# Performance work log

Hardware: AMD Instinct MI355X
Metric: run time of the kernel (lower is better)

## Reference

```python
import jax, jax.numpy as jnp
import numpy as np

B, N, DIM, PDIM, H, DH, M, CDIM = 1, 48, 256, 128, 8, 64, 128, 512
INNER = H * DH
EPS = 1e-5


def setup_inputs() -> dict:
    key = jax.random.key(0)
    ks = jax.random.split(key, 40)
    def w(k, shape):
        return jax.random.normal(k, shape, jnp.float32) * 0.02
    inp = {
        "singles": jax.random.normal(ks[0], (B, N, DIM), jnp.float32),
        "pairs": jax.random.normal(ks[1], (B, N, N, PDIM), jnp.float32),
        "ligand_emb": jax.random.normal(ks[2], (B, M, CDIM), jnp.float32),
        "mask": jnp.ones((B, N), dtype=bool),
        "rotary_pos": jax.random.normal(ks[3], (1, 1, 1, DH), jnp.float32),
        "ln_s_g": jnp.ones((DIM,)), "ln_s_b": jnp.zeros((DIM,)),
        "ln_p_g": jnp.ones((PDIM,)), "ln_p_b": jnp.zeros((PDIM,)),
        "sa_qkv": w(ks[4], (DIM, 3 * INNER)),
        "sa_out_w": w(ks[5], (INNER, DIM)), "sa_out_b": jnp.zeros((DIM,)),
        "sff_w1": w(ks[6], (DIM, 4 * DIM)), "sff_b1": jnp.zeros((4 * DIM,)),
        "sff_w2": w(ks[7], (4 * DIM, DIM)), "sff_b2": jnp.zeros((DIM,)),
        "pa_qkv": w(ks[8], (PDIM, 3 * INNER)),
        "pa_out_w": w(ks[9], (INNER, PDIM)), "pa_out_b": jnp.zeros((PDIM,)),
        "pff_w1": w(ks[10], (PDIM, 4 * PDIM)), "pff_b1": jnp.zeros((4 * PDIM,)),
        "pff_w2": w(ks[11], (4 * PDIM, PDIM)), "pff_b2": jnp.zeros((PDIM,)),
        "ca_q": w(ks[12], (PDIM, INNER)),
        "ca_kv": w(ks[13], (CDIM, 2 * INNER)),
        "ca_out_w": w(ks[14], (INNER, PDIM)), "ca_out_b": jnp.zeros((PDIM,)),
        "s2p_w": w(ks[15], (DIM, PDIM)), "s2p_b": jnp.zeros((PDIM,)),
        "p2s_w": w(ks[16], (PDIM, DIM)), "p2s_b": jnp.zeros((DIM,)),
    }
    return inp


def _rotate_half(x):
    shp = x.shape
    xr = x.reshape(shp[:-1] + (shp[-1] // 2, 2))
    x1, x2 = xr[..., 0], xr[..., 1]
    return jnp.stack((-x2, x1), axis=-1).reshape(shp)


def _rope(pos, t):
    return t * jnp.cos(pos) + _rotate_half(t) * jnp.sin(pos)


def _split_heads(t):
    b, n, _ = t.shape
    return t.reshape(b, n, H, DH).transpose(0, 2, 1, 3)  # b h n d


def _merge_heads(t):
    b, h, n, d = t.shape
    return t.transpose(0, 2, 1, 3).reshape(b, n, h * d)


def _layer_norm(x, g, b):
    m = jnp.mean(x, axis=-1, keepdims=True)
    v = jnp.mean(jnp.square(x - m), axis=-1, keepdims=True)
    return (x - m) * jax.lax.rsqrt(v + EPS) * g + b


def _mish(x):
    return x * jnp.tanh(jax.nn.softplus(x))


def _attn_core(q, k, v, key_mask=None):
    dots = jnp.einsum('bhid,bhjd->bhij', q, k) * (DH ** -0.5)
    if key_mask is not None:
        neg = -jnp.finfo(dots.dtype).max
        dots = jnp.where(key_mask[:, None, None, :], dots, neg)
    a = jax.nn.softmax(dots, axis=-1)
    return jnp.einsum('bhij,bhjd->bhid', a, v)


def _self_attn(x, w_qkv, w_out, b_out, rotary_pos, key_mask=None):
    q, k, v = jnp.split(x @ w_qkv, 3, axis=-1)
    q, k, v = _split_heads(q), _split_heads(k), _split_heads(v)
    q, k = _rope(rotary_pos, q), _rope(rotary_pos, k)
    out = _merge_heads(_attn_core(q, k, v, key_mask))
    return out @ w_out + b_out


def _cross_attn(x, ctx, w_q, w_kv, w_out, b_out, rotary_pos):
    q = _split_heads(x @ w_q)
    k, v = jnp.split(ctx @ w_kv, 2, axis=-1)
    k, v = _split_heads(k), _split_heads(v)
    q, k = _rope(rotary_pos, q), _rope(rotary_pos, k)
    out = _merge_heads(_attn_core(q, k, v))
    return out @ w_out + b_out


def _ff(x, w1, b1, w2, b2):
    return _mish(x @ w1 + b1) @ w2 + b2


def _forward(singles, pairs, ligand_emb, mask, rotary_pos,
             ln_s_g, ln_s_b, ln_p_g, ln_p_b,
             sa_qkv, sa_out_w, sa_out_b, sff_w1, sff_b1, sff_w2, sff_b2,
             pa_qkv, pa_out_w, pa_out_b, pff_w1, pff_b1, pff_w2, pff_b2,
             ca_q, ca_kv, ca_out_w, ca_out_b, s2p_w, s2p_b, p2s_w, p2s_b):
    # single track
    s_norm = _layer_norm(singles, ln_s_g, ln_s_b)
    singles = singles + _self_attn(s_norm, sa_qkv, sa_out_w, sa_out_b, rotary_pos, mask)
    singles = singles + _ff(singles, sff_w1, sff_b1, sff_w2, sff_b2)
    # pair track: flatten i*j into one long sequence
    b, i, j, d = pairs.shape
    p_norm = _layer_norm(pairs, ln_p_g, ln_p_b)
    p_flat = p_norm.reshape(b, i * j, d)
    p_attn = _self_attn(p_flat, pa_qkv, pa_out_w, pa_out_b, rotary_pos, None)
    pairs = pairs + p_attn.reshape(b, i, j, d)
    # ligand cross attention (on pre-norm pairs, as in source)
    p_cross = _cross_attn(p_flat, ligand_emb, ca_q, ca_kv, ca_out_w, ca_out_b, rotary_pos)
    pairs = pairs + p_cross.reshape(b, i, j, d)
    pairs = pairs + _ff(pairs, pff_w1, pff_b1, pff_w2, pff_b2)
    # cross-track communication
    single_contrib = singles @ s2p_w + s2p_b              # [b,n,pdim]
    pair_contrib = jnp.mean(pairs, axis=2) @ p2s_w + p2s_b  # [b,n,dim]
    pairs = pairs + single_contrib[:, None, :, :] + single_contrib[:, :, None, :]
    singles = singles + pair_contrib
    return singles, pairs


def reference(singles, pairs, ligand_emb, mask, rotary_pos,
              ln_s_g, ln_s_b, ln_p_g, ln_p_b,
              sa_qkv, sa_out_w, sa_out_b, sff_w1, sff_b1, sff_w2, sff_b2,
              pa_qkv, pa_out_w, pa_out_b, pff_w1, pff_b1, pff_w2, pff_b2,
              ca_q, ca_kv, ca_out_w, ca_out_b, s2p_w, s2p_b, p2s_w, p2s_b):
    return _forward(singles, pairs, ligand_emb, mask, rotary_pos,
                    ln_s_g, ln_s_b, ln_p_g, ln_p_b,
                    sa_qkv, sa_out_w, sa_out_b, sff_w1, sff_b1, sff_w2, sff_b2,
                    pa_qkv, pa_out_w, pa_out_b, pff_w1, pff_b1, pff_w2, pff_b2,
                    ca_q, ca_kv, ca_out_w, ca_out_b, s2p_w, s2p_b, p2s_w, p2s_b)
```

## Files before the change

### kernel.cpp

```cpp
#include <hip/hip_runtime.h>
#include <math.h>

#define EPS 1e-5f

typedef __attribute__((ext_vector_type(8))) short short8;
typedef __attribute__((ext_vector_type(4))) short short4v;
typedef __attribute__((ext_vector_type(4))) float float4v;

__device__ inline short f2bf(float f) {
  union { float f; unsigned u; } c; c.f = f;
  unsigned u = c.u;
  u += 0x7FFF + ((u >> 16) & 1);
  return (short)(u >> 16);
}

struct TransDesc { const float* src; short* dst; int K; int N; int tile0; };
struct TransArgs { TransDesc d[13]; int nd; };

__global__ __launch_bounds__(256) void prep_kernel(
    TransArgs args, int tiles, int ln_end,
    const float* __restrict__ xs, const float* __restrict__ gs,
    const float* __restrict__ bs, float* __restrict__ ys,
    const float* __restrict__ xp, const float* __restrict__ gp,
    const float* __restrict__ bp, float* __restrict__ yp,
    float* __restrict__ zbase) {
  int bid = blockIdx.x;
  int tid = threadIdx.x;
  if (bid < tiles) {
    __shared__ float tile[32][33];
    int wi = 0;
    while (wi + 1 < args.nd && args.d[wi + 1].tile0 <= bid) ++wi;
    TransDesc de = args.d[wi];
    int lt = bid - de.tile0;
    int ntx = de.N / 32;
    int k0 = (lt / ntx) * 32, n0 = (lt % ntx) * 32;
    int tx = tid & 31, ty = tid >> 5;
#pragma unroll
    for (int yy = 0; yy < 4; ++yy) {
      int kk = ty + yy * 8;
      tile[kk][tx] = de.src[(size_t)(k0 + kk) * de.N + n0 + tx];
    }
    __syncthreads();
#pragma unroll
    for (int yy = 0; yy < 4; ++yy) {
      int nn = ty + yy * 8;
      de.dst[(size_t)(n0 + nn) * de.K + k0 + tx] = f2bf(tile[tx][nn]);
    }
    return;
  }
  if (bid < ln_end) {
    __shared__ float red[256];
    int row = bid - tiles;
    const float *x, *g, *b;
    float* y;
    int D;
    if (row < 48) { x = xs; g = gs; b = bs; y = ys; D = 256; }
    else { row -= 48; x = xp; g = gp; b = bp; y = yp; D = 128; }
    const float* xr = x + (size_t)row * D;
    float* yr = y + (size_t)row * D;
    float s = (tid < D) ? xr[tid] : 0.f;
    red[tid] = s; __syncthreads();
    for (int st = 128; st > 0; st >>= 1) {
      if (tid < st) red[tid] += red[tid + st];
      __syncthreads();
    }
    float mean = red[0] / D;
    __syncthreads();
    float v = 0.f;
    if (tid < D) { float t = xr[tid] - mean; v = t * t; }
    red[tid] = v; __syncthreads();
    for (int st = 128; st > 0; st >>= 1) {
      if (tid < st) red[tid] += red[tid + st];
      __syncthreads();
    }
    float rstd = rsqrtf(red[0] / D + EPS);
    if (tid < D) yr[tid] = (xr[tid] - mean) * rstd * g[tid] + b[tid];
    return;
  }
  size_t i4 = ((size_t)(bid - ln_end) * 256 + tid) * 4;
  *(float4*)(zbase + i4) = make_float4(0.f, 0.f, 0.f, 0.f);
}

struct ProjJob {
  const float* A; const short* Wt;
  int M, K, N;
  short *Qd, *Kd, *Vd;
  int rowspad, vld, qend, kend, tile0;
  float qscale;
};
struct ProjArgs { ProjJob j[4]; int nj; };

__global__ __launch_bounds__(256) void proj_kernel(
    ProjArgs args, const float* __restrict__ rope_pos) {
  __shared__ short As[64][72];
  __shared__ short Ws[64][72];
  int t = blockIdx.x;
  int ji = 0;
  while (ji + 1 < args.nj && args.j[ji + 1].tile0 <= t) ++ji;
  ProjJob jb = args.j[ji];
  int lt = t - jb.tile0;
  int ntx = jb.N / 64;
  int m0 = (lt / ntx) * 64, n0 = (lt % ntx) * 64;
  int tid = threadIdx.x;
  int wave = tid >> 6, lane = tid & 63;
  int n16 = lane & 15, quad = lane >> 4;
  float4v acc[4];
#pragma unroll
  for (int f = 0; f < 4; ++f) acc[f] = (float4v){0.f, 0.f, 0.f, 0.f};

  for (int k0 = 0; k0 < jb.K; k0 += 64) {
    __syncthreads();
    for (int idx = tid; idx < 1024; idx += 256) {
      int row = idx >> 4, c4 = (idx & 15) * 4;
      float4 av = make_float4(0.f, 0.f, 0.f, 0.f);
      if (m0 + row < jb.M)
        av = *(const float4*)(jb.A + (size_t)(m0 + row) * jb.K + k0 + c4);
      short4v s;
      s.x = f2bf(av.x); s.y = f2bf(av.y); s.z = f2bf(av.z); s.w = f2bf(av.w);
      *(short4v*)&As[row][c4] = s;
    }
    for (int idx = tid; idx < 512; idx += 256) {
      int row = idx >> 3, kc = (idx & 7) * 8;
      short8 w = *(const short8*)(jb.Wt + (size_t)(n0 + row) * jb.K + k0 + kc);
      *(short8*)&Ws[row][kc] = w;
    }
    __syncthreads();
#pragma unroll
    for (int s = 0; s < 2; ++s) {
      short8 a = *(const short8*)&As[wave * 16 + n16][s * 32 + quad * 8];
#pragma unroll
      for (int f = 0; f < 4; ++f) {
        short8 b = *(const short8*)&Ws[f * 16 + n16][s * 32 + quad * 8];
        acc[f] = __builtin_amdgcn_mfma_f32_16x16x32_bf16(a, b, acc[f], 0, 0, 0);
      }
    }
  }

#pragma unroll
  for (int f = 0; f < 4; ++f) {
    int col = n0 + f * 16 + n16;
    if (col < jb.kend) {
      int rel = (col < jb.qend) ? col : col - jb.qend;
      int hh = rel >> 6, d = col & 63;
      float pv = rope_pos[d];
      float cp = cosf(pv), sp = sinf(pv);
      float sc = (col < jb.qend) ? jb.qscale : 1.f;
      short* dst = (col < jb.qend) ? jb.Qd : jb.Kd;
#pragma unroll
      for (int r = 0; r < 4; ++r) {
        float x = acc[f][r];
        float xp = __shfl_xor(x, 1);
        float o = (n16 & 1) ? (x * cp + xp * sp) : (x * cp - xp * sp);
        int row = m0 + wave * 16 + quad * 4 + r;
        if (row < jb.M)
          dst[((size_t)hh * jb.rowspad + row) * 64 + d] = f2bf(o * sc);
      }
    } else {
      int vcol = col - jb.kend;
      int hh = vcol >> 6, d = vcol & 63;
      short4v s;
#pragma unroll
      for (int r = 0; r < 4; ++r) ((short*)&s)[r] = f2bf(acc[f][r]);
      int j0 = m0 + wave * 16 + quad * 4;
      if (j0 < jb.M)
        *(short4v*)(jb.Vd + (size_t)(hh * 64 + d) * jb.vld + j0) = s;
    }
  }
}

struct FJob {
  const short *Q, *K, *V;
  int nkpad;
  float* O;
  float* Lsum;
  int nq, nk, ns, nqt, blk0;
};
struct FArgs { FJob j[3]; int nj; };

__global__ __launch_bounds__(256) void fattn_kernel(FArgs args) {
  __shared__ short Ks[64][72];
  __shared__ short Vs[64][72];
  __shared__ short Ps[4][16][72];
  int bid = blockIdx.x;
  int ji = 0;
  while (ji + 1 < args.nj && args.j[ji + 1].blk0 <= bid) ++ji;
  FJob jb = args.j[ji];
  int local = bid - jb.blk0;
  int h = local & 7;
  int rest = local >> 3;
  int qt = rest % jb.nqt;
  int z = rest / jb.nqt;
  int nqpad = jb.nqt * 64;
  int q0 = qt * 64;
  int nkpad = jb.nkpad, nk = jb.nk;
  int tid = threadIdx.x;
  int wave = tid >> 6, lane = tid & 63;
  int n16 = lane & 15, quad = lane >> 4;

  int ntiles = nkpad >> 6;
  int tiles_per = (ntiles + jb.ns - 1) / jb.ns;
  int kbeg = z * tiles_per * 64;
  int kend = min(nkpad, kbeg + tiles_per * 64);

  const short* kb = jb.K + (size_t)h * nkpad * 64;
  const short* vt = jb.V + (size_t)h * 64 * nkpad;
  const short* qr = jb.Q + (size_t)h * nqpad * 64 +
                    (size_t)(q0 + wave * 16 + n16) * 64;
  short8 a0 = *(const short8*)(qr + quad * 8);
  short8 a1 = *(const short8*)(qr + 32 + quad * 8);

  float4v Of[4];
#pragma unroll
  for (int f = 0; f < 4; ++f) Of[f] = (float4v){0.f, 0.f, 0.f, 0.f};
  float l_par[4] = {0.f, 0.f, 0.f, 0.f};

  int r0 = tid >> 3, cc0 = (tid & 7) * 8;
  int r1 = (tid + 256) >> 3, cc1 = ((tid + 256) & 7) * 8;

  short8 pK0 = *(const short8*)(kb + (size_t)(kbeg + r0) * 64 + cc0);
  short8 pK1 = *(const short8*)(kb + (size_t)(kbeg + r1) * 64 + cc1);
  short8 pV0 = *(const short8*)(vt + (size_t)r0 * nkpad + kbeg + cc0);
  short8 pV1 = *(const short8*)(vt + (size_t)r1 * nkpad + kbeg + cc1);

  for (int kt0 = kbeg; kt0 < kend; kt0 += 64) {
    __syncthreads();
    *(short8*)&Ks[r0][cc0] = pK0;
    *(short8*)&Ks[r1][cc1] = pK1;
    *(short8*)&Vs[r0][cc0] = pV0;
    *(short8*)&Vs[r1][cc1] = pV1;
    int nxt = kt0 + 64;
    if (nxt < kend) {
      pK0 = *(const short8*)(kb + (size_t)(nxt + r0) * 64 + cc0);
      pK1 = *(const short8*)(kb + (size_t)(nxt + r1) * 64 + cc1);
      pV0 = *(const short8*)(vt + (size_t)r0 * nkpad + nxt + cc0);
      pV1 = *(const short8*)(vt + (size_t)r1 * nkpad + nxt + cc1);
    }
    __syncthreads();

    float4v Sf[4];
#pragma unroll
    for (int f = 0; f < 4; ++f) {
      short8 b0 = *(const short8*)&Ks[f * 16 + n16][quad * 8];
      short8 b1 = *(const short8*)&Ks[f * 16 + n16][32 + quad * 8];
      float4v a = (float4v){0.f, 0.f, 0.f, 0.f};
      a = __builtin_amdgcn_mfma_f32_16x16x32_bf16(a0, b0, a, 0, 0, 0);
      a = __builtin_amdgcn_mfma_f32_16x16x32_bf16(a1, b1, a, 0, 0, 0);
      Sf[f] = a;
    }
    if (kt0 + 64 > nk) {
#pragma unroll
      for (int f = 0; f < 4; ++f) {
        int j = kt0 + f * 16 + n16;
        if (j >= nk) {
          Sf[f][0] = -1e30f; Sf[f][1] = -1e30f;
          Sf[f][2] = -1e30f; Sf[f][3] = -1e30f;
        }
      }
    }
    float p[4][4];
#pragma unroll
    for (int r = 0; r < 4; ++r) {
      float t = 0.f;
#pragma unroll
      for (int f = 0; f < 4; ++f) {
        float e = __expf(Sf[f][r]);
        p[f][r] = e;
        t += e;
      }
      l_par[r] += t;
    }
#pragma unroll
    for (int f = 0; f < 4; ++f)
#pragma unroll
      for (int r = 0; r < 4; ++r)
        Ps[wave][quad * 4 + r][f * 16 + n16] = f2bf(p[f][r]);
#pragma unroll
    for (int s = 0; s < 2; ++s) {
      short8 pa = *(const short8*)&Ps[wave][n16][s * 32 + quad * 8];
#pragma unroll
      for (int f = 0; f < 4; ++f) {
        short8 vb = *(const short8*)&Vs[f * 16 + n16][s * 32 + quad * 8];
        Of[f] = __builtin_amdgcn_mfma_f32_16x16x32_bf16(pa, vb, Of[f], 0, 0, 0);
      }
    }
  }

  float l[4];
#pragma unroll
  for (int r = 0; r < 4; ++r) {
    float t = l_par[r];
    t += __shfl_xor(t, 1);
    t += __shfl_xor(t, 2);
    t += __shfl_xor(t, 4);
    t += __shfl_xor(t, 8);
    l[r] = t;
  }

  if (jb.ns == 1) {
#pragma unroll
    for (int r = 0; r < 4; ++r) {
      int row = q0 + wave * 16 + quad * 4 + r;
      if (row >= jb.nq) continue;
      float inv = 1.f / l[r];
#pragma unroll
      for (int f = 0; f < 4; ++f)
        jb.O[(size_t)row * 512 + h * 64 + f * 16 + n16] = Of[f][r] * inv;
    }
  } else {
#pragma unroll
    for (int r = 0; r < 4; ++r) {
      int row = q0 + wave * 16 + quad * 4 + r;
#pragma unroll
      for (int f = 0; f < 4; ++f)
        atomicAdd(&jb.O[(size_t)row * 512 + h * 64 + f * 16 + n16], Of[f][r]);
      if (n16 == 0) atomicAdd(&jb.Lsum[(size_t)h * jb.nq + row], l[r]);
    }
  }
}

struct TJob {
  int type;
  const float *A1, *A2;
  const short *W1, *W2;
  const float *b1, *b2, *resid, *normL;
  float *C, *pmean;
  short* Ct;
  int M, K1, K2, N, nz, mish, dual, tile0;
};
struct TArgs { TJob j[4]; int nj; };

__global__ __launch_bounds__(256) void tjobs_kernel(TArgs args) {
  __shared__ short As[32][136];
  __shared__ short Ws[32][136];
  int t = blockIdx.x;
  int ji = 0;
  while (ji + 1 < args.nj && args.j[ji + 1].tile0 <= t) ++ji;
  TJob jb = args.j[ji];
  int lt = t - jb.tile0;
  int tid = threadIdx.x;

  if (jb.type == 2) {
    int idx = lt * 256 + tid;
    int d = idx & 127;
    int j = (idx >> 7) % 48;
    int i = idx / (48 * 128);
    jb.C[idx] = jb.A1[idx] + jb.A2[j * 128 + d] + jb.A2[i * 128 + d];
    return;
  }
  if (jb.type == 4) {
    if (tid < 128) {
      float acc = jb.b1[tid];
      for (int m = 0; m < jb.K1; ++m)
        acc += jb.A1[m] * jb.resid[(size_t)m * 128 + tid];
      jb.C[tid] = acc;
    }
    return;
  }

  int ntx = jb.N / 32, nmt = (jb.M + 31) >> 5;
  int per_z = ntx * nmt;
  int z = lt / per_z, rem = lt - z * per_z;
  int m0 = (rem / ntx) * 32, n0 = (rem % ntx) * 32;
  int wave = tid >> 6, lane = tid & 63;
  int n16 = lane & 15, quad = lane >> 4;
  int mrow = (wave >> 1) * 16, ncol = (wave & 1) * 16;
  float4v acc = (float4v){0.f, 0.f, 0.f, 0.f};
  int Ktot = jb.K1 + (jb.dual ? jb.K2 : 0);
  int chunk = Ktot / jb.nz;
  int kst = z * chunk, ken = kst + chunk;
  for (int kc = kst; kc < ken; kc += 128) {
    __syncthreads();
    for (int idx = tid; idx < 1024; idx += 256) {
      int row = idx >> 5, c4 = (idx & 31) * 4;
      int k = kc + c4;
      float4 av = make_float4(0.f, 0.f, 0.f, 0.f);
      if (m0 + row < jb.M) {
        if (!jb.dual || k < jb.K1) {
          av = *(const float4*)(jb.A1 + (size_t)(m0 + row) * jb.K1 + k);
          if (jb.normL) {
            float inv = 1.f / jb.normL[(size_t)(k >> 6) * jb.M + m0 + row];
            av.x *= inv; av.y *= inv; av.z *= inv; av.w *= inv;
          }
        } else {
          av = *(const float4*)(jb.A2 + (size_t)(m0 + row) * jb.K2 +
                                (k - jb.K1));
        }
      }
      short4v s;
      s.x = f2bf(av.x); s.y = f2bf(av.y); s.z = f2bf(av.z); s.w = f2bf(av.w);
      *(short4v*)&As[row][c4] = s;
    }
    for (int idx = tid; idx < 512; idx += 256) {
      int row = idx >> 4, k8 = (idx & 15) * 8;
      int k = kc + k8;
      const short* src = (jb.dual && k >= jb.K1)
          ? (jb.W2 + (size_t)(n0 + row) * jb.K2 + (k - jb.K1))
          : (jb.W1 + (size_t)(n0 + row) * jb.K1 + k);
      *(short8*)&Ws[row][k8] = *(const short8*)src;
    }
    __syncthreads();
#pragma unroll
    for (int ks = 0; ks < 4; ++ks) {
      short8 a = *(const short8*)&As[mrow + n16][ks * 32 + quad * 8];
      short8 b = *(const short8*)&Ws[ncol + n16][ks * 32 + quad * 8];
      acc = __builtin_amdgcn_mfma_f32_16x16x32_bf16(a, b, acc, 0, 0, 0);
    }
  }
  int col = n0 + ncol + n16;
  if (jb.Ct) {
    short4v s;
#pragma unroll
    for (int r = 0; r < 4; ++r) ((short*)&s)[r] = f2bf(acc[r]);
    int rbase = m0 + mrow + quad * 4;
    *(short4v*)(jb.Ct + (size_t)col * jb.M + rbase) = s;
    return;
  }
  if (jb.nz == 1) {
#pragma unroll
    for (int r = 0; r < 4; ++r) {
      int row = m0 + mrow + quad * 4 + r;
      if (row >= jb.M) continue;
      float v = acc[r];
      if (jb.b1) v += jb.b1[col];
      if (jb.b2) v += jb.b2[col];
      if (jb.mish) {
        float sp = (v > 20.f) ? v : log1pf(expf(v));
        v = v * tanhf(sp);
      }
      if (jb.resid) v += jb.resid[(size_t)row * jb.N + col];
      jb.C[(size_t)row * jb.N + col] = v;
      if (jb.pmean) atomicAdd(&jb.pmean[(row / 48) * 128 + col], v * (1.f / 48.f));
    }
  } else {
#pragma unroll
    for (int r = 0; r < 4; ++r) {
      int row = m0 + mrow + quad * 4 + r;
      if (row >= jb.M) continue;
      float v = acc[r];
      if (z == 0) {
        if (jb.b1) v += jb.b1[col];
        if (jb.b2) v += jb.b2[col];
        if (jb.resid) v += jb.resid[(size_t)row * jb.N + col];
      }
      atomicAdd(&jb.C[(size_t)row * jb.N + col], v);
      if (jb.pmean) atomicAdd(&jb.pmean[(row / 48) * 128 + col], v * (1.f / 48.f));
    }
  }
}

extern "C" void kernel_launch(void* const* d_in, const int* in_sizes, int n_in,
                              void* d_out, int out_size, void* d_ws, size_t ws_size,
                              hipStream_t stream) {
  (void)in_sizes; (void)n_in; (void)out_size; (void)ws_size;
  const float* singles = (const float*)d_in[0];
  const float* pairs   = (const float*)d_in[1];
  const float* ligand  = (const float*)d_in[2];
  const float* rotary  = (const float*)d_in[4];
  const float* ln_s_g  = (const float*)d_in[5];
  const float* ln_s_b  = (const float*)d_in[6];
  const float* ln_p_g  = (const float*)d_in[7];
  const float* ln_p_b  = (const float*)d_in[8];
  const float* sa_out_b= (const float*)d_in[11];
  const float* sff_b1  = (const float*)d_in[13];
  const float* sff_w2f = (const float*)d_in[14];
  const float* sff_b2  = (const float*)d_in[15];
  const float* pa_out_b= (const float*)d_in[18];
  const float* pff_b1  = (const float*)d_in[20];
  const float* pff_b2  = (const float*)d_in[22];
  const float* ca_out_b= (const float*)d_in[26];
  const float* s2p_wf  = (const float*)d_in[27];
  const float* s2p_b   = (const float*)d_in[28];
  const float* p2s_b   = (const float*)d_in[30];

  float* ws = (float*)d_ws;
  size_t off = 0;
  auto alloc = [&](size_t n) { float* p = ws + off; off += n; return p; };
  float* s_norm   = alloc(12288);
  float* p_norm   = alloc(294912);
  float* attn_s   = alloc(24576);
  float* h1_s     = alloc(49152);
  float* attn_c   = alloc(1179648);
  float* attn_p   = alloc(1179648);
  float* Lsum     = alloc(18432);
  float* pairs2   = alloc(294912);
  float* pairs3   = alloc(294912);
  float* singles1 = alloc(12288);
  float* singles2 = alloc(12288);
  float* sc_buf   = alloc(6144);
  float* pmean    = alloc(6144);
  const size_t zero_floats = 1824768;
  float* bc       = alloc(128);
  short* Wct      = (short*)alloc(65536);
  short* wt       = (short*)alloc(1081344);
  short* Qb       = (short*)alloc(589824);
  short* Kb       = (short*)alloc(589824);
  short* Vtb      = (short*)alloc(589824);
  short* Qcb      = (short*)alloc(589824);
  short* Kcb      = (short*)alloc(32768);
  short* Vcb      = (short*)alloc(32768);
  short* Qsb      = (short*)alloc(16384);
  short* Ksb      = (short*)alloc(16384);
  short* Vsb      = (short*)alloc(16384);

  float* out_s = (float*)d_out;
  float* out_p = (float*)d_out + 12288;

  struct WSpec { const float* src; int K, N; };
  WSpec specs[13] = {
    {(const float*)d_in[9], 256, 1536}, {(const float*)d_in[10], 512, 256},
    {(const float*)d_in[12], 256, 1024}, {sff_w2f, 1024, 256},
    {(const float*)d_in[16], 128, 1536}, {(const float*)d_in[17], 512, 128},
    {(const float*)d_in[19], 128, 512}, {(const float*)d_in[21], 512, 128},
    {(const float*)d_in[23], 128, 512}, {(const float*)d_in[24], 512, 1024},
    {(const float*)d_in[25], 512, 128}, {s2p_wf, 256, 128},
    {(const float*)d_in[29], 128, 256}};
  TransArgs ta;
  ta.nd = 13;
  short* wptr[13];
  int tiles = 0;
  size_t woff = 0;
  for (int i = 0; i < 13; ++i) {
    ta.d[i].src = specs[i].src;
    ta.d[i].dst = wt + woff;
    ta.d[i].K = specs[i].K;
    ta.d[i].N = specs[i].N;
    ta.d[i].tile0 = tiles;
    wptr[i] = wt + woff;
    woff += (size_t)specs[i].K * specs[i].N;
    tiles += (specs[i].K / 32) * (specs[i].N / 32);
  }

  const float scale = 0.125f;
  const int NS = 4;

  {
    int ln_end = tiles + 48 + 2304;
    int zero_blocks = (int)(zero_floats / 1024);
    hipLaunchKernelGGL(prep_kernel, dim3(ln_end + zero_blocks), dim3(256), 0,
                       stream, ta, tiles, ln_end,
                       singles, ln_s_g, ln_s_b, s_norm,
                       pairs, ln_p_g, ln_p_b, p_norm, attn_p);
  }

  {
    ProjArgs pa;
    pa.nj = 4;
    int t0 = 0;
    auto setj = [&](int i, const float* A, const short* Wt, int M, int K,
                    int N, short* Qd, short* Kd, short* Vd, int rowspad,
                    int vld, int qend, int kend, float qscale) {
      pa.j[i] = {A, Wt, M, K, N, Qd, Kd, Vd, rowspad, vld, qend, kend, t0,
                 qscale};
      t0 += (N / 64) * ((M + 63) / 64);
    };
    setj(0, s_norm, wptr[0], 48, 256, 1536, Qsb, Ksb, Vsb, 64, 64, 512, 1024,
         scale);
    setj(1, p_norm, wptr[4], 2304, 128, 1536, Qb, Kb, Vtb, 2304, 2304, 512,
         1024, scale);
    setj(2, p_norm, wptr[8], 2304, 128, 512, Qcb, nullptr, nullptr, 2304, 0,
         512, 512, scale);
    setj(3, ligand, wptr[9], 128, 512, 1024, nullptr, Kcb, Vcb, 128, 128, 0,
         512, 1.f);
    hipLaunchKernelGGL(proj_kernel, dim3(t0), dim3(256), 0, stream, pa, rotary);
  }

  {
    FArgs fa;
    fa.nj = 3;
    fa.j[0] = {Qb, Kb, Vtb, 2304, attn_p, Lsum, 2304, 2304, NS, 36, 0};
    fa.j[1] = {Qsb, Ksb, Vsb, 64, attn_s, nullptr, 48, 48, 1, 1, 8 * 36 * NS};
    fa.j[2] = {Qcb, Kcb, Vcb, 128, attn_c, nullptr, 2304, 128, 1, 36,
               8 * 36 * NS + 8};
    hipLaunchKernelGGL(fattn_kernel, dim3(8 * 36 * NS + 8 + 8 * 36), dim3(256),
                       0, stream, fa);
  }

  auto gemm_tiles = [](int M, int N, int nz) {
    return (N / 32) * ((M + 31) / 32) * nz;
  };
  TJob jz{};

  {
    TArgs tj; tj.nj = 4;
    TJob a = jz;
    a.type = 0; a.A1 = attn_p; a.A2 = attn_c; a.W1 = wptr[5]; a.W2 = wptr[10];
    a.b1 = pa_out_b; a.b2 = ca_out_b; a.resid = pairs; a.normL = Lsum;
    a.C = pairs2; a.M = 2304; a.K1 = 512; a.K2 = 512; a.N = 128; a.nz = 4;
    a.dual = 1; a.tile0 = 0;
    int t1 = gemm_tiles(2304, 128, 4);
    TJob b = jz;
    b.type = 0; b.A1 = attn_s; b.W1 = wptr[1]; b.b1 = sa_out_b;
    b.resid = singles; b.C = singles1; b.M = 48; b.K1 = 512; b.N = 256;
    b.nz = 2; b.tile0 = t1;
    int t2 = t1 + gemm_tiles(48, 256, 2);
    TJob c = jz;
    c.type = 0; c.A1 = sff_w2f; c.W1 = wptr[11]; c.Ct = Wct;
    c.M = 1024; c.K1 = 256; c.N = 128; c.nz = 1; c.tile0 = t2;
    int t3 = t2 + gemm_tiles(1024, 128, 1);
    TJob d = jz;
    d.type = 4; d.A1 = sff_b2; d.b1 = s2p_b; d.resid = s2p_wf; d.C = bc;
    d.K1 = 256; d.tile0 = t3;
    tj.j[0] = a; tj.j[1] = b; tj.j[2] = c; tj.j[3] = d;
    hipLaunchKernelGGL(tjobs_kernel, dim3(t3 + 1), dim3(256), 0, stream, tj);
  }
  {
    TArgs tj; tj.nj = 2;
    TJob a = jz;
    a.type = 0; a.A1 = pairs2; a.W1 = wptr[6]; a.b1 = pff_b1; a.mish = 1;
    a.C = attn_c ; a.M = 2304; a.K1 = 128; a.N = 512; a.nz = 1;
    a.tile0 = 0;
    int t1 = gemm_tiles(2304, 512, 1);
    TJob b = jz;
    b.type = 0; b.A1 = singles1; b.W1 = wptr[2]; b.b1 = sff_b1; b.mish = 1;
    b.C = h1_s; b.M = 48; b.K1 = 256; b.N = 1024; b.nz = 1; b.tile0 = t1;
    tj.j[0] = a; tj.j[1] = b;
    hipLaunchKernelGGL(tjobs_kernel, dim3(t1 + gemm_tiles(48, 1024, 1)),
                       dim3(256), 0, stream, tj);
  }
  {
    TArgs tj; tj.nj = 3;
    TJob a = jz;
    a.type = 0; a.A1 = attn_c ; a.W1 = wptr[7]; a.b1 = pff_b2;
    a.resid = pairs2; a.C = pairs3; a.pmean = pmean;
    a.M = 2304; a.K1 = 512; a.N = 128; a.nz = 2; a.tile0 = 0;
    int t1 = gemm_tiles(2304, 128, 2);
    TJob b = jz;
    b.type = 0; b.A1 = h1_s; b.W1 = wptr[3]; b.b1 = sff_b2; b.resid = singles1;
    b.C = singles2; b.M = 48; b.K1 = 1024; b.N = 256; b.nz = 2; b.tile0 = t1;
    int t2 = t1 + gemm_tiles(48, 256, 2);
    TJob c = jz;
    c.type = 0; c.A1 = singles1; c.A2 = h1_s; c.W1 = wptr[11]; c.W2 = Wct;
    c.b1 = bc; c.C = sc_buf; c.M = 48; c.K1 = 256; c.K2 = 1024; c.N = 128;
    c.nz = 2; c.dual = 1; c.tile0 = t2;
    tj.j[0] = a; tj.j[1] = b; tj.j[2] = c;
    hipLaunchKernelGGL(tjobs_kernel, dim3(t2 + gemm_tiles(48, 128, 2)),
                       dim3(256), 0, stream, tj);
  }
  {
    TArgs tj; tj.nj = 2;
    TJob a = jz;
    a.type = 0; a.A1 = pmean; a.W1 = wptr[12]; a.b1 = p2s_b;
    a.resid = singles2; a.C = out_s; a.M = 48; a.K1 = 128; a.N = 256;
    a.nz = 1; a.tile0 = 0;
    int t1 = gemm_tiles(48, 256, 1);
    TJob b = jz;
    b.type = 2; b.A1 = pairs3; b.A2 = sc_buf; b.C = out_p; b.tile0 = t1;
    tj.j[0] = a; tj.j[1] = b;
    hipLaunchKernelGGL(tjobs_kernel, dim3(t1 + 1152), dim3(256), 0, stream, tj);
  }
}
```

Before: 288.9 us.

## Replace split-KV atomic accumulation with bf16 partial buffers and combine pass

The pair-attention split-KV blocks now write unnormalized bf16 partial outputs and row sums into per-split buffers instead of issuing fp32 atomicAdds into a zeroed output. A new combine job sums the partials and normalizes. The out-projection GEMMs shift one launch later, which adds an extra kernel launch. Separately, the pair-mean atomics are pre-reduced across each wave with shuffles so each column issues one atomic, and the large zero-init region shrinks. The trade-off is lower precision in the partials plus extra memory traffic and a launch, in exchange for removing heavy atomic contention and memset work.

Result: no change. 287.6 us (-0.4%).

```diff
diff --git a/kernel.cpp b/kernel.cpp
--- a/kernel.cpp
+++ b/kernel.cpp
@@ -12,6 +12,11 @@
   unsigned u = c.u;
   u += 0x7FFF + ((u >> 16) & 1);
   return (short)(u >> 16);
+}
+__device__ inline float bf2f(short s) {
+  union { unsigned u; float f; } c;
+  c.u = ((unsigned)(unsigned short)s) << 16;
+  return c.f;
 }
 
 struct TransDesc { const float* src; short* dst; int K; int N; int tile0; };
@@ -172,7 +177,7 @@
   const short *Q, *K, *V;
   int nkpad;
   float* O;
-  float* Lsum;
+  short* Opart; float* Lpart;
   int nq, nk, ns, nqt, blk0;
 };
 struct FArgs { FJob j[3]; int nj; };
@@ -307,13 +312,15 @@
         jb.O[(size_t)row * 512 + h * 64 + f * 16 + n16] = Of[f][r] * inv;
     }
   } else {
+    size_t pbase = ((size_t)(h * jb.nqt + qt) * jb.ns + z);
+    short* op = jb.Opart + pbase * 4096;
 #pragma unroll
     for (int r = 0; r < 4; ++r) {
-      int row = q0 + wave * 16 + quad * 4 + r;
+      int rl = wave * 16 + quad * 4 + r;
 #pragma unroll
       for (int f = 0; f < 4; ++f)
-        atomicAdd(&jb.O[(size_t)row * 512 + h * 64 + f * 16 + n16], Of[f][r]);
-      if (n16 == 0) atomicAdd(&jb.Lsum[(size_t)h * jb.nq + row], l[r]);
+        op[(size_t)rl * 64 + f * 16 + n16] = f2bf(Of[f][r]);
+      if (n16 == 0) jb.Lpart[pbase * 64 + rl] = l[r];
     }
   }
 }
@@ -322,7 +329,7 @@
   int type;
   const float *A1, *A2;
   const short *W1, *W2;
-  const float *b1, *b2, *resid, *normL;
+  const float *b1, *b2, *resid, *L;
   float *C, *pmean;
   short* Ct;
   int M, K1, K2, N, nz, mish, dual, tile0;
@@ -353,6 +360,35 @@
       for (int m = 0; m < jb.K1; ++m)
         acc += jb.A1[m] * jb.resid[(size_t)m * 128 + tid];
       jb.C[tid] = acc;
+    }
+    return;
+  }
+  if (jb.type == 5) {
+    int h = lt / jb.M, qt = lt % jb.M;
+    int q = tid >> 2, d0 = (tid & 3) * 16;
+    size_t base = (size_t)(h * jb.M + qt) * jb.nz;
+    float l = 0.f;
+    for (int s = 0; s < jb.nz; ++s) l += jb.L[(base + s) * 64 + q];
+    float inv = 1.f / l;
+    float acc[16];
+#pragma unroll
+    for (int i = 0; i < 16; ++i) acc[i] = 0.f;
+    for (int s = 0; s < jb.nz; ++s) {
+      const short* op = jb.Ct + (base + s) * 4096 + q * 64 + d0;
+#pragma unroll
+      for (int c = 0; c < 2; ++c) {
+        short8 v = *(const short8*)(op + c * 8);
+#pragma unroll
+        for (int j = 0; j < 8; ++j) acc[c * 8 + j] += bf2f(v[j]);
+      }
+    }
+    int row = qt * 64 + q;
+    float* dst = jb.C + (size_t)row * 512 + h * 64 + d0;
+#pragma unroll
+    for (int c = 0; c < 4; ++c) {
+      float4 o = make_float4(acc[c * 4] * inv, acc[c * 4 + 1] * inv,
+                             acc[c * 4 + 2] * inv, acc[c * 4 + 3] * inv);
+      *(float4*)(dst + c * 4) = o;
     }
     return;
   }
@@ -375,16 +411,11 @@
       int k = kc + c4;
       float4 av = make_float4(0.f, 0.f, 0.f, 0.f);
       if (m0 + row < jb.M) {
-        if (!jb.dual || k < jb.K1) {
+        if (!jb.dual || k < jb.K1)
           av = *(const float4*)(jb.A1 + (size_t)(m0 + row) * jb.K1 + k);
-          if (jb.normL) {
-            float inv = 1.f / jb.normL[(size_t)(k >> 6) * jb.M + m0 + row];
-            av.x *= inv; av.y *= inv; av.z *= inv; av.w *= inv;
-          }
-        } else {
+        else
           av = *(const float4*)(jb.A2 + (size_t)(m0 + row) * jb.K2 +
                                 (k - jb.K1));
-        }
       }
       short4v s;
       s.x = f2bf(av.x); s.y = f2bf(av.y); s.z = f2bf(av.z); s.w = f2bf(av.w);
@@ -415,6 +446,7 @@
     *(short4v*)(jb.Ct + (size_t)col * jb.M + rbase) = s;
     return;
   }
+  float tsum = 0.f;
   if (jb.nz == 1) {
 #pragma unroll
     for (int r = 0; r < 4; ++r) {
@@ -429,7 +461,7 @@
       }
       if (jb.resid) v += jb.resid[(size_t)row * jb.N + col];
       jb.C[(size_t)row * jb.N + col] = v;
-      if (jb.pmean) atomicAdd(&jb.pmean[(row / 48) * 128 + col], v * (1.f / 48.f));
+      tsum += v;
     }
   } else {
 #pragma unroll
@@ -443,8 +475,15 @@
         if (jb.resid) v += jb.resid[(size_t)row * jb.N + col];
       }
       atomicAdd(&jb.C[(size_t)row * jb.N + col], v);
-      if (jb.pmean) atomicAdd(&jb.pmean[(row / 48) * 128 + col], v * (1.f / 48.f));
-    }
+      tsum += v;
+    }
+  }
+  if (jb.pmean) {
+    tsum *= (1.f / 48.f);
+    tsum += __shfl_xor(tsum, 16);
+    tsum += __shfl_xor(tsum, 32);
+    if (quad == 0)
+      atomicAdd(&jb.pmean[((m0 + mrow) / 48) * 128 + col], tsum);
   }
 }
 
@@ -479,18 +518,19 @@
   float* p_norm   = alloc(294912);
   float* attn_s   = alloc(24576);
   float* h1_s     = alloc(49152);
+  float* attn_p   = alloc(294912);
   float* attn_c   = alloc(1179648);
-  float* attn_p   = alloc(1179648);
-  float* Lsum     = alloc(18432);
   float* pairs2   = alloc(294912);
   float* pairs3   = alloc(294912);
   float* singles1 = alloc(12288);
   float* singles2 = alloc(12288);
   float* sc_buf   = alloc(6144);
   float* pmean    = alloc(6144);
-  const size_t zero_floats = 1824768;
+  const size_t zero_floats = 626688;
   float* bc       = alloc(128);
   short* Wct      = (short*)alloc(65536);
+  float* Lpart    = alloc(73728);
+  short* OpartS   = (short*)alloc(2359296);
   short* wt       = (short*)alloc(1081344);
   short* Qb       = (short*)alloc(589824);
   short* Kb       = (short*)alloc(589824);
@@ -539,7 +579,7 @@
     hipLaunchKernelGGL(prep_kernel, dim3(ln_end + zero_blocks), dim3(256), 0,
                        stream, ta, tiles, ln_end,
                        singles, ln_s_g, ln_s_b, s_norm,
-                       pairs, ln_p_g, ln_p_b, p_norm, attn_p);
+                       pairs, ln_p_g, ln_p_b, p_norm, pairs2);
   }
 
   {
@@ -567,9 +607,10 @@
   {
     FArgs fa;
     fa.nj = 3;
-    fa.j[0] = {Qb, Kb, Vtb, 2304, attn_p, Lsum, 2304, 2304, NS, 36, 0};
-    fa.j[1] = {Qsb, Ksb, Vsb, 64, attn_s, nullptr, 48, 48, 1, 1, 8 * 36 * NS};
-    fa.j[2] = {Qcb, Kcb, Vcb, 128, attn_c, nullptr, 2304, 128, 1, 36,
+    fa.j[0] = {Qb, Kb, Vtb, 2304, attn_p, OpartS, Lpart, 2304, 2304, NS, 36, 0};
+    fa.j[1] = {Qsb, Ksb, Vsb, 64, attn_s, nullptr, nullptr, 48, 48, 1, 1,
+               8 * 36 * NS};
+    fa.j[2] = {Qcb, Kcb, Vcb, 128, attn_c, nullptr, nullptr, 2304, 128, 1, 36,
                8 * 36 * NS + 8};
     hipLaunchKernelGGL(fattn_kernel, dim3(8 * 36 * NS + 8 + 8 * 36), dim3(256),
                        0, stream, fa);
@@ -583,11 +624,9 @@
   {
     TArgs tj; tj.nj = 4;
     TJob a = jz;
-    a.type = 0; a.A1 = attn_p; a.A2 = attn_c; a.W1 = wptr[5]; a.W2 = wptr[10];
-    a.b1 = pa_out_b; a.b2 = ca_out_b; a.resid = pairs; a.normL = Lsum;
-    a.C = pairs2; a.M = 2304; a.K1 = 512; a.K2 = 512; a.N = 128; a.nz = 4;
-    a.dual = 1; a.tile0 = 0;
-    int t1 = gemm_tiles(2304, 128, 4);
+    a.type = 5; a.Ct = OpartS; a.L = Lpart; a.C = attn_p; a.M = 36; a.nz = NS;
+    a.tile0 = 0;
+    int t1 = 8 * 36;
     TJob b = jz;
     b.type = 0; b.A1 = attn_s; b.W1 = wptr[1]; b.b1 = sa_out_b;
     b.resid = singles; b.C = singles1; b.M = 48; b.K1 = 512; b.N = 256;
@@ -606,10 +645,11 @@
   {
     TArgs tj; tj.nj = 2;
     TJob a = jz;
-    a.type = 0; a.A1 = pairs2; a.W1 = wptr[6]; a.b1 = pff_b1; a.mish = 1;
-    a.C = attn_c ; a.M = 2304; a.K1 = 128; a.N = 512; a.nz = 1;
+    a.type = 0; a.A1 = attn_p; a.A2 = attn_c; a.W1 = wptr[5]; a.W2 = wptr[10];
+    a.b1 = pa_out_b; a.b2 = ca_out_b; a.resid = pairs; a.C = pairs2;
+    a.M = 2304; a.K1 = 512; a.K2 = 512; a.N = 128; a.nz = 4; a.dual = 1;
     a.tile0 = 0;
-    int t1 = gemm_tiles(2304, 512, 1);
+    int t1 = gemm_tiles(2304, 128, 4);
     TJob b = jz;
     b.type = 0; b.A1 = singles1; b.W1 = wptr[2]; b.b1 = sff_b1; b.mish = 1;
     b.C = h1_s; b.M = 48; b.K1 = 256; b.N = 1024; b.nz = 1; b.tile0 = t1;
@@ -620,10 +660,10 @@
   {
     TArgs tj; tj.nj = 3;
     TJob a = jz;
-    a.type = 0; a.A1 = attn_c ; a.W1 = wptr[7]; a.b1 = pff_b2;
-    a.resid = pairs2; a.C = pairs3; a.pmean = pmean;
-    a.M = 2304; a.K1 = 512; a.N = 128; a.nz = 2; a.tile0 = 0;
-    int t1 = gemm_tiles(2304, 128, 2);
+    a.type = 0; a.A1 = pairs2; a.W1 = wptr[6]; a.b1 = pff_b1; a.mish = 1;
+    a.C = attn_c ; a.M = 2304; a.K1 = 128; a.N = 512; a.nz = 1;
+    a.tile0 = 0;
+    int t1 = gemm_tiles(2304, 512, 1);
     TJob b = jz;
     b.type = 0; b.A1 = h1_s; b.W1 = wptr[3]; b.b1 = sff_b2; b.resid = singles1;
     b.C = singles2; b.M = 48; b.K1 = 1024; b.N = 256; b.nz = 2; b.tile0 = t1;
@@ -637,6 +677,16 @@
                        dim3(256), 0, stream, tj);
   }
   {
+    TArgs tj; tj.nj = 1;
+    TJob a = jz;
+    a.type = 0; a.A1 = attn_c ; a.W1 = wptr[7]; a.b1 = pff_b2;
+    a.resid = pairs2; a.C = pairs3; a.pmean = pmean;
+    a.M = 2304; a.K1 = 512; a.N = 128; a.nz = 2; a.tile0 = 0;
+    tj.j[0] = a;
+    hipLaunchKernelGGL(tjobs_kernel, dim3(gemm_tiles(2304, 128, 2)),
+                       dim3(256), 0, stream, tj);
+  }
+  {
     TArgs tj; tj.nj = 2;
     TJob a = jz;
     a.type = 0; a.A1 = pmean; a.W1 = wptr[12]; a.b1 = p2s_b;
```
